# Kernel tuning notes

Hardware: AMD Instinct MI355X
Metric: run time of the kernel (lower is better)

## Reference

```python
import jax, jax.numpy as jnp
import numpy as np

N_NODES = 50000
SEQ_LEN = 32
N_TOKENS = 100000
EMB_DIM = 128          # in_feats / 2
IN_FEATS = 256
N_HIDDEN = 256
N_CLASSES = 40
N_EDGES = 800000
PAD_IX = 0


def setup_inputs() -> dict:
    key = jax.random.key(0)
    k1, k2, k3, k4, k5, k6 = jax.random.split(key, 6)
    features = jax.random.randint(k1, (N_NODES, SEQ_LEN), 0, N_TOKENS, dtype=jnp.int32)
    src = jax.random.randint(k2, (N_EDGES,), 0, N_NODES, dtype=jnp.int32)
    dst = jax.random.randint(k3, (N_EDGES,), 0, N_NODES, dtype=jnp.int32)
    emb_table = jax.random.normal(k4, (N_TOKENS, EMB_DIM), dtype=jnp.float32) * 0.02
    W1 = jax.random.normal(k5, (IN_FEATS, N_HIDDEN), dtype=jnp.float32) * 0.02
    b1 = jnp.zeros((N_HIDDEN,), dtype=jnp.float32)
    W2 = jax.random.normal(k6, (N_HIDDEN, N_CLASSES), dtype=jnp.float32) * 0.02
    b2 = jnp.zeros((N_CLASSES,), dtype=jnp.float32)
    return {"features": features, "src": src, "dst": dst,
            "emb_table": emb_table, "W1": W1, "b1": b1, "W2": W2, "b2": b2}


def _apply_embs(features, emb_table):
    # padding_idx row contributes zeros (nn.Embedding padding_idx semantics)
    emb = emb_table.at[PAD_IX].set(0.0)
    h = emb[features]                                    # [N, L, D]
    seq_len = jnp.sum(features != PAD_IX, axis=1)        # [N]
    seq_len = jnp.maximum(seq_len, 1)[:, None].astype(h.dtype)
    h1 = h.sum(axis=1) / seq_len                         # masked mean
    h2 = h.max(axis=1)                                   # max pool (pads are 0)
    return jnp.concatenate((h1, h2), axis=1)             # [N, 2D]


def _graph_conv(h, src, dst, norm_s, norm_d, W, b):
    # DGL GraphConv, norm='both': out = D_in^{-1/2} A D_out^{-1/2} h W + b
    hw = h @ W                                           # transform first (smaller msgs)
    m = (hw * norm_s[:, None])[src]                      # gather messages [E, F]
    agg = jax.ops.segment_sum(m, dst, num_segments=N_NODES)
    return agg * norm_d[:, None] + b


def reference(features, src, dst, emb_table, W1, b1, W2, b2):
    ones_e = jnp.ones((src.shape[0],), dtype=jnp.float32)
    deg_out = jnp.maximum(jax.ops.segment_sum(ones_e, src, num_segments=N_NODES), 1.0)
    deg_in = jnp.maximum(jax.ops.segment_sum(ones_e, dst, num_segments=N_NODES), 1.0)
    norm_s = deg_out ** -0.5
    norm_d = deg_in ** -0.5

    h = _apply_embs(features, emb_table)                 # [N, in_feats]
    h = jax.nn.relu(_graph_conv(h, src, dst, norm_s, norm_d, W1, b1))
    # dropout is identity in eval mode
    h = _graph_conv(h, src, dst, norm_s, norm_d, W2, b2)
    return h                                             # [N, n_classes]
```

## Files before the change

kernel.cpp:

```cpp
#include <hip/hip_runtime.h>
#include <math.h>

#define N_NODES 50000
#define SEQ_LEN 32
#define EMB_DIM 128
#define IN_FEATS 256
#define N_HIDDEN 256
#define N_CLASSES 40
#define N_EDGES 800000
#define N_TOKENS 100000

#define SLOT 64
#define NBIN 196
#define BINCAP 4608
#define EPB 4000

typedef short short8 __attribute__((ext_vector_type(8)));
typedef float f32x4 __attribute__((ext_vector_type(4)));

__device__ __forceinline__ unsigned short f2bf(float x) {
  unsigned int u = __float_as_uint(x);
  unsigned int r = (u + 0x7FFFu + ((u >> 16) & 1u)) >> 16;
  return (unsigned short)r;
}
__device__ __forceinline__ float bf2f(unsigned short s) {
  return __uint_as_float((unsigned int)s << 16);
}
__device__ __forceinline__ unsigned int pack2bf(float a, float b) {
  return (unsigned int)f2bf(a) | ((unsigned int)f2bf(b) << 16);
}

__global__ __launch_bounds__(256) void k_prep(const float* __restrict__ emb,
                                              unsigned short* __restrict__ emb_b,
                                              const float* __restrict__ W1,
                                              unsigned short* __restrict__ Wp1,
                                              const float* __restrict__ W2,
                                              unsigned short* __restrict__ Wp2) {
  int b = blockIdx.x, tid = threadIdx.x;
  if (b < 2048) {
    const int total = N_TOKENS * EMB_DIM / 4;
    for (int i = b * 256 + tid; i < total; i += 2048 * 256) {
      float4 v = ((const float4*)emb)[i];
      ushort4 o;
      o.x = f2bf(v.x); o.y = f2bf(v.y); o.z = f2bf(v.z); o.w = f2bf(v.w);
      ((ushort4*)emb_b)[i] = o;
    }
  } else if (b < 2080) {
    int g = (b - 2048) * 256 + tid;
    int lane = g & 63, jb = (g >> 6) & 15, kt = g >> 10;
    int col = jb * 16 + (lane & 15);
    int kbase = kt * 32 + (lane >> 4) * 8;
    unsigned short* o = Wp1 + (size_t)g * 8;
    #pragma unroll
    for (int e = 0; e < 8; ++e) o[e] = f2bf(W1[(size_t)(kbase + e) * N_HIDDEN + col]);
  } else {
    int g = (b - 2080) * 256 + tid;
    if (g < 8 * 3 * 64) {
      int lane = g & 63, jb = (g >> 6) % 3, kt = g / (3 * 64);
      int col = jb * 16 + (lane & 15);
      int kbase = kt * 32 + (lane >> 4) * 8;
      unsigned short* o = Wp2 + (size_t)g * 8;
      #pragma unroll
      for (int e = 0; e < 8; ++e)
        o[e] = (col < N_CLASSES) ? f2bf(W2[(size_t)(kbase + e) * N_CLASSES + col]) : (unsigned short)0;
    }
  }
}

__global__ __launch_bounds__(256) void k_binA(const int* __restrict__ src,
                                              const int* __restrict__ dst,
                                              int* __restrict__ gcntD,
                                              int* __restrict__ gcntS,
                                              unsigned int* __restrict__ dbin,
                                              unsigned char* __restrict__ sbin) {
  __shared__ int cntD[NBIN], cntS[NBIN], baseD[NBIN], baseS[NBIN];
  int tid = threadIdx.x;
  if (tid < NBIN) { cntD[tid] = 0; cntS[tid] = 0; }
  __syncthreads();
  int e0 = blockIdx.x * EPB;
  for (int j = tid; j < EPB; j += 256) {
    int d = dst[e0 + j], s = src[e0 + j];
    atomicAdd(&cntD[d >> 8], 1);
    atomicAdd(&cntS[s >> 8], 1);
  }
  __syncthreads();
  if (tid < NBIN) {
    baseD[tid] = atomicAdd(&gcntD[tid], cntD[tid]);
    baseS[tid] = atomicAdd(&gcntS[tid], cntS[tid]);
    cntD[tid] = 0;
    cntS[tid] = 0;
  }
  __syncthreads();
  for (int j = tid; j < EPB; j += 256) {
    int d = dst[e0 + j], s = src[e0 + j];
    int bd = d >> 8, bs = s >> 8;
    int od = atomicAdd(&cntD[bd], 1);
    int pd = baseD[bd] + od;
    if (pd < BINCAP) dbin[(size_t)bd * BINCAP + pd] = ((unsigned int)s << 8) | (unsigned int)(d & 255);
    int os = atomicAdd(&cntS[bs], 1);
    int ps = baseS[bs] + os;
    if (ps < BINCAP) sbin[(size_t)bs * BINCAP + ps] = (unsigned char)(s & 255);
  }
}

__global__ __launch_bounds__(256) void k_binB(const unsigned int* __restrict__ dbin,
                                              const int* __restrict__ gcntD,
                                              int* __restrict__ cursor,
                                              int* __restrict__ csr_pad) {
  __shared__ int cnt[256];
  int tid = threadIdx.x, b = blockIdx.x;
  cnt[tid] = 0;
  __syncthreads();
  int n = min(gcntD[b], BINCAP);
  const unsigned int* bb = dbin + (size_t)b * BINCAP;
  for (int j = tid; j < n; j += 256) {
    unsigned int e = bb[j];
    int lo = e & 255;
    int slot = atomicAdd(&cnt[lo], 1);
    if (slot < SLOT) csr_pad[(size_t)(b * 256 + lo) * SLOT + slot] = (int)(e >> 8);
  }
  __syncthreads();
  int node = b * 256 + tid;
  if (node < N_NODES) cursor[node] = min(cnt[tid], SLOT);
}

__global__ __launch_bounds__(256) void k_degoutnorm(const unsigned char* __restrict__ sbin,
                                                    const int* __restrict__ gcntS,
                                                    const int* __restrict__ cursor,
                                                    float* __restrict__ norm_s,
                                                    float* __restrict__ norm_d) {
  __shared__ int cnt[256];
  int tid = threadIdx.x, b = blockIdx.x;
  cnt[tid] = 0;
  __syncthreads();
  int n = min(gcntS[b], BINCAP);
  const unsigned char* bb = sbin + (size_t)b * BINCAP;
  for (int j = tid; j < n; j += 256) atomicAdd(&cnt[bb[j]], 1);
  __syncthreads();
  int node = b * 256 + tid;
  if (node < N_NODES) {
    norm_s[node] = 1.0f / sqrtf((float)max(cnt[tid], 1));
    norm_d[node] = 1.0f / sqrtf((float)max(cursor[node], 1));
  }
}

__global__ __launch_bounds__(256) void k_embed(const int* __restrict__ feats,
                                               const uint4* __restrict__ rows4,
                                               uint4* __restrict__ h4) {
  int tid = threadIdx.x;
  int w = tid >> 6, lane = tid & 63;
  int node = blockIdx.x * 4 + w;
  int lq = lane & 15, qg = lane >> 4;
  int laneL = lane & 31;

  int tok0 = feats[(size_t)node * SEQ_LEN + laneL];
  unsigned long long m = __ballot(tok0 != 0);
  int cnt = (int)__popcll(m & 0xFFFFFFFFull);
  float inv = 1.0f / (float)max(cnt, 1);

  float s0 = 0.f, s1 = 0.f, s2 = 0.f, s3 = 0.f, s4 = 0.f, s5 = 0.f, s6 = 0.f, s7 = 0.f;
  float m0 = -INFINITY, m1 = -INFINITY, m2 = -INFINITY, m3 = -INFINITY;
  float m4 = -INFINITY, m5 = -INFINITY, m6 = -INFINITY, m7 = -INFINITY;
  #pragma unroll
  for (int t = 0; t < 8; ++t) {
    int tok = __shfl(tok0, t * 4 + qg);
    uint4 v = make_uint4(0u, 0u, 0u, 0u);
    if (tok) v = rows4[(size_t)tok * 16 + lq];
    float f0 = bf2f((unsigned short)(v.x & 0xFFFF)), f1 = bf2f((unsigned short)(v.x >> 16));
    float f2 = bf2f((unsigned short)(v.y & 0xFFFF)), f3 = bf2f((unsigned short)(v.y >> 16));
    float f4 = bf2f((unsigned short)(v.z & 0xFFFF)), f5 = bf2f((unsigned short)(v.z >> 16));
    float f6 = bf2f((unsigned short)(v.w & 0xFFFF)), f7 = bf2f((unsigned short)(v.w >> 16));
    s0 += f0; s1 += f1; s2 += f2; s3 += f3; s4 += f4; s5 += f5; s6 += f6; s7 += f7;
    m0 = fmaxf(m0, f0); m1 = fmaxf(m1, f1); m2 = fmaxf(m2, f2); m3 = fmaxf(m3, f3);
    m4 = fmaxf(m4, f4); m5 = fmaxf(m5, f5); m6 = fmaxf(m6, f6); m7 = fmaxf(m7, f7);
  }
  #pragma unroll
  for (int mask = 16; mask <= 32; mask <<= 1) {
    s0 += __shfl_xor(s0, mask); s1 += __shfl_xor(s1, mask);
    s2 += __shfl_xor(s2, mask); s3 += __shfl_xor(s3, mask);
    s4 += __shfl_xor(s4, mask); s5 += __shfl_xor(s5, mask);
    s6 += __shfl_xor(s6, mask); s7 += __shfl_xor(s7, mask);
    m0 = fmaxf(m0, __shfl_xor(m0, mask)); m1 = fmaxf(m1, __shfl_xor(m1, mask));
    m2 = fmaxf(m2, __shfl_xor(m2, mask)); m3 = fmaxf(m3, __shfl_xor(m3, mask));
    m4 = fmaxf(m4, __shfl_xor(m4, mask)); m5 = fmaxf(m5, __shfl_xor(m5, mask));
    m6 = fmaxf(m6, __shfl_xor(m6, mask)); m7 = fmaxf(m7, __shfl_xor(m7, mask));
  }
  if (qg == 0) {
    uint4* hv = h4 + (size_t)node * 32;
    hv[lq] = make_uint4(pack2bf(s0 * inv, s1 * inv), pack2bf(s2 * inv, s3 * inv),
                        pack2bf(s4 * inv, s5 * inv), pack2bf(s6 * inv, s7 * inv));
    hv[16 + lq] = make_uint4(pack2bf(m0, m1), pack2bf(m2, m3),
                             pack2bf(m4, m5), pack2bf(m6, m7));
  }
}

__global__ __launch_bounds__(256) void k_mm1(const unsigned short* __restrict__ hb,
                                             const unsigned short* __restrict__ Wp,
                                             const float* __restrict__ norm_s,
                                             unsigned short* __restrict__ out) {
  __shared__ unsigned short sA[64 * 256];
  int tid = threadIdx.x;
  int r0 = blockIdx.x * 64;
  #pragma unroll
  for (int it = 0; it < 8; ++it) {
    int idx = it * 256 + tid;
    int r = idx >> 5, kb = idx & 31;
    uint4 v = make_uint4(0, 0, 0, 0);
    int row = r0 + r;
    if (row < N_NODES) v = *(const uint4*)(hb + (size_t)row * 256 + kb * 8);
    *(uint4*)&sA[r * 256 + ((kb ^ (r & 7)) << 3)] = v;
  }
  __syncthreads();

  int w = tid >> 6, lane = tid & 63;
  const short8* W8 = (const short8*)Wp;
  f32x4 acc[4][4];
  #pragma unroll
  for (int i = 0; i < 4; ++i)
    #pragma unroll
    for (int j = 0; j < 4; ++j) acc[i][j] = (f32x4){0.f, 0.f, 0.f, 0.f};

  #pragma unroll
  for (int kt = 0; kt < 8; ++kt) {
    short8 a[4], b[4];
    int kb = kt * 4 + (lane >> 4);
    #pragma unroll
    for (int ri = 0; ri < 4; ++ri) {
      int r = ri * 16 + (lane & 15);
      a[ri] = *(const short8*)&sA[r * 256 + ((kb ^ (r & 7)) << 3)];
    }
    #pragma unroll
    for (int jb = 0; jb < 4; ++jb) b[jb] = W8[(kt * 16 + w * 4 + jb) * 64 + lane];
    #pragma unroll
    for (int ri = 0; ri < 4; ++ri)
      #pragma unroll
      for (int jb = 0; jb < 4; ++jb)
        acc[ri][jb] = __builtin_amdgcn_mfma_f32_16x16x32_bf16(a[ri], b[jb], acc[ri][jb], 0, 0, 0);
  }

  #pragma unroll
  for (int ri = 0; ri < 4; ++ri) {
    #pragma unroll
    for (int rr = 0; rr < 4; ++rr) {
      int row = r0 + ri * 16 + (lane >> 4) * 4 + rr;
      if (row < N_NODES) {
        float ns = norm_s[row];
        #pragma unroll
        for (int jb = 0; jb < 4; ++jb) {
          int col = w * 64 + jb * 16 + (lane & 15);
          out[(size_t)row * 256 + col] = f2bf(acc[ri][jb][rr] * ns);
        }
      }
    }
  }
}

__global__ __launch_bounds__(256) void k_agg1(const uint4* __restrict__ rows4,
                                              const int* __restrict__ cursor,
                                              const int* __restrict__ csr_pad,
                                              const float* __restrict__ norm_d,
                                              const float* __restrict__ b1,
                                              uint4* __restrict__ out4) {
  int tid = threadIdx.x;
  int w = tid >> 6, lane = tid & 63;
  int node = blockIdx.x * 4 + w;
  int cnt = __builtin_amdgcn_readfirstlane(cursor[node]);
  const int* csr = csr_pad + (size_t)node * SLOT;
  int half = lane >> 5, lq = lane & 31;

  float a0 = 0.f, a1 = 0.f, a2 = 0.f, a3 = 0.f, a4 = 0.f, a5 = 0.f, a6 = 0.f, a7 = 0.f;
  int e = 0;
  for (; e + 8 <= cnt; e += 8) {
    int s0 = csr[e + 0 + half], s1 = csr[e + 2 + half];
    int s2 = csr[e + 4 + half], s3 = csr[e + 6 + half];
    uint4 v0 = rows4[(size_t)s0 * 32 + lq];
    uint4 v1 = rows4[(size_t)s1 * 32 + lq];
    uint4 v2 = rows4[(size_t)s2 * 32 + lq];
    uint4 v3 = rows4[(size_t)s3 * 32 + lq];
    #pragma unroll
    for (int i = 0; i < 4; ++i) {
      uint4 v = (i == 0) ? v0 : (i == 1) ? v1 : (i == 2) ? v2 : v3;
      a0 += bf2f((unsigned short)(v.x & 0xFFFF)); a1 += bf2f((unsigned short)(v.x >> 16));
      a2 += bf2f((unsigned short)(v.y & 0xFFFF)); a3 += bf2f((unsigned short)(v.y >> 16));
      a4 += bf2f((unsigned short)(v.z & 0xFFFF)); a5 += bf2f((unsigned short)(v.z >> 16));
      a6 += bf2f((unsigned short)(v.w & 0xFFFF)); a7 += bf2f((unsigned short)(v.w >> 16));
    }
  }
  for (; e + 2 <= cnt; e += 2) {
    int s = csr[e + half];
    uint4 v = rows4[(size_t)s * 32 + lq];
    a0 += bf2f((unsigned short)(v.x & 0xFFFF)); a1 += bf2f((unsigned short)(v.x >> 16));
    a2 += bf2f((unsigned short)(v.y & 0xFFFF)); a3 += bf2f((unsigned short)(v.y >> 16));
    a4 += bf2f((unsigned short)(v.z & 0xFFFF)); a5 += bf2f((unsigned short)(v.z >> 16));
    a6 += bf2f((unsigned short)(v.w & 0xFFFF)); a7 += bf2f((unsigned short)(v.w >> 16));
  }
  if (e < cnt) {
    uint4 v = make_uint4(0u, 0u, 0u, 0u);
    if (half == 0) v = rows4[(size_t)csr[e] * 32 + lq];
    a0 += bf2f((unsigned short)(v.x & 0xFFFF)); a1 += bf2f((unsigned short)(v.x >> 16));
    a2 += bf2f((unsigned short)(v.y & 0xFFFF)); a3 += bf2f((unsigned short)(v.y >> 16));
    a4 += bf2f((unsigned short)(v.z & 0xFFFF)); a5 += bf2f((unsigned short)(v.z >> 16));
    a6 += bf2f((unsigned short)(v.w & 0xFFFF)); a7 += bf2f((unsigned short)(v.w >> 16));
  }
  a0 += __shfl_xor(a0, 32); a1 += __shfl_xor(a1, 32);
  a2 += __shfl_xor(a2, 32); a3 += __shfl_xor(a3, 32);
  a4 += __shfl_xor(a4, 32); a5 += __shfl_xor(a5, 32);
  a6 += __shfl_xor(a6, 32); a7 += __shfl_xor(a7, 32);

  if (half == 0) {
    float nd = norm_d[node];
    float4 bb0 = *(const float4*)&b1[8 * lq];
    float4 bb1 = *(const float4*)&b1[8 * lq + 4];
    float o0 = fmaxf(a0 * nd + bb0.x, 0.f), o1 = fmaxf(a1 * nd + bb0.y, 0.f);
    float o2 = fmaxf(a2 * nd + bb0.z, 0.f), o3 = fmaxf(a3 * nd + bb0.w, 0.f);
    float o4 = fmaxf(a4 * nd + bb1.x, 0.f), o5 = fmaxf(a5 * nd + bb1.y, 0.f);
    float o6 = fmaxf(a6 * nd + bb1.z, 0.f), o7 = fmaxf(a7 * nd + bb1.w, 0.f);
    out4[(size_t)node * 32 + lq] = make_uint4(pack2bf(o0, o1), pack2bf(o2, o3),
                                              pack2bf(o4, o5), pack2bf(o6, o7));
  }
}

__global__ __launch_bounds__(256) void k_mm2(const unsigned short* __restrict__ h2b,
                                             const unsigned short* __restrict__ Wp,
                                             const float* __restrict__ norm_s,
                                             unsigned short* __restrict__ out) {
  __shared__ unsigned short sA[64 * 256];
  int tid = threadIdx.x;
  int r0 = blockIdx.x * 64;
  #pragma unroll
  for (int it = 0; it < 8; ++it) {
    int idx = it * 256 + tid;
    int r = idx >> 5, kb = idx & 31;
    uint4 v = make_uint4(0, 0, 0, 0);
    int row = r0 + r;
    if (row < N_NODES) v = *(const uint4*)(h2b + (size_t)row * 256 + kb * 8);
    *(uint4*)&sA[r * 256 + ((kb ^ (r & 7)) << 3)] = v;
  }
  __syncthreads();

  int w = tid >> 6, lane = tid & 63;
  const short8* W8 = (const short8*)Wp;
  f32x4 acc[3];
  #pragma unroll
  for (int j = 0; j < 3; ++j) acc[j] = (f32x4){0.f, 0.f, 0.f, 0.f};

  #pragma unroll
  for (int kt = 0; kt < 8; ++kt) {
    int r = w * 16 + (lane & 15);
    int kb = kt * 4 + (lane >> 4);
    short8 a = *(const short8*)&sA[r * 256 + ((kb ^ (r & 7)) << 3)];
    #pragma unroll
    for (int jb = 0; jb < 3; ++jb) {
      short8 b = W8[(kt * 3 + jb) * 64 + lane];
      acc[jb] = __builtin_amdgcn_mfma_f32_16x16x32_bf16(a, b, acc[jb], 0, 0, 0);
    }
  }

  #pragma unroll
  for (int rr = 0; rr < 4; ++rr) {
    int row = r0 + w * 16 + (lane >> 4) * 4 + rr;
    if (row < N_NODES) {
      float ns = norm_s[row];
      #pragma unroll
      for (int jb = 0; jb < 3; ++jb) {
        int col = jb * 16 + (lane & 15);
        if (col < N_CLASSES) out[(size_t)row * N_CLASSES + col] = f2bf(acc[jb][rr] * ns);
      }
    }
  }
}

__global__ __launch_bounds__(256) void k_agg2(const unsigned int* __restrict__ rows,
                                              const int* __restrict__ cursor,
                                              const int* __restrict__ csr_pad,
                                              const float* __restrict__ norm_d,
                                              const float* __restrict__ b2,
                                              float* __restrict__ out) {
  int tid = threadIdx.x;
  int w = tid >> 6, lane = tid & 63;
  int node = blockIdx.x * 4 + w;
  int slot = lane / 20, fl = lane % 20;
  int cnt = __builtin_amdgcn_readfirstlane(cursor[node]);
  const int* csr = csr_pad + (size_t)node * SLOT;

  float a0 = 0.f, a1 = 0.f;
  if (slot < 3) {
    for (int e = slot; e < cnt; e += 3) {
      int s = csr[e];
      unsigned int v = rows[(size_t)s * 20 + fl];
      a0 += bf2f((unsigned short)(v & 0xFFFF));
      a1 += bf2f((unsigned short)(v >> 16));
    }
  }
  float p0 = __shfl(a0, lane + 20), p1 = __shfl(a1, lane + 20);
  float q0 = __shfl(a0, lane + 40), q1 = __shfl(a1, lane + 40);
  if (slot == 0) {
    a0 += p0 + q0; a1 += p1 + q1;
    float nd = norm_d[node];
    float o0 = a0 * nd + b2[2 * fl];
    float o1 = a1 * nd + b2[2 * fl + 1];
    *(float2*)&out[(size_t)node * N_CLASSES + 2 * fl] = make_float2(o0, o1);
  }
}

extern "C" void kernel_launch(void* const* d_in, const int* in_sizes, int n_in,
                              void* d_out, int out_size, void* d_ws, size_t ws_size,
                              hipStream_t stream) {
  const int*   feats = (const int*)d_in[0];
  const int*   src   = (const int*)d_in[1];
  const int*   dst   = (const int*)d_in[2];
  const float* emb   = (const float*)d_in[3];
  const float* W1    = (const float*)d_in[4];
  const float* b1    = (const float*)d_in[5];
  const float* W2    = (const float*)d_in[6];
  const float* b2    = (const float*)d_in[7];
  float* out = (float*)d_out;

  char* base = (char*)d_ws;
  size_t off = 0;
  auto alloc = [&](size_t bytes) -> char* {
    char* p = base + off;
    off += (bytes + 255) & ~(size_t)255;
    return p;
  };
  unsigned short* hb      = (unsigned short*)alloc((size_t)N_NODES * IN_FEATS * 2);
  unsigned short* msgb    = (unsigned short*)alloc((size_t)N_NODES * N_HIDDEN * 2);
  unsigned short* hw2b    = (unsigned short*)alloc((size_t)N_NODES * N_CLASSES * 2);
  unsigned short* emb_b   = (unsigned short*)alloc((size_t)N_TOKENS * EMB_DIM * 2);
  unsigned short* Wp1     = (unsigned short*)alloc((size_t)8 * 16 * 64 * 8 * 2);
  unsigned short* Wp2     = (unsigned short*)alloc((size_t)8 * 3 * 64 * 8 * 2);
  int*   gcnt    = (int*)alloc((size_t)512 * 4);
  int*   gcntD   = gcnt;
  int*   gcntS   = gcnt + 256;
  int*   cursor  = (int*)alloc((size_t)N_NODES * 4);
  float* norm_s  = (float*)alloc((size_t)N_NODES * 4);
  float* norm_d  = (float*)alloc((size_t)N_NODES * 4);
  unsigned int*  dbin = (unsigned int*)alloc((size_t)NBIN * BINCAP * 4);
  unsigned char* sbin = (unsigned char*)alloc((size_t)NBIN * BINCAP);
  int*   csr_pad = (int*)alloc((size_t)N_NODES * SLOT * 4);

  hipMemsetAsync(gcnt, 0, 512 * 4, stream);

  k_prep<<<2086, 256, 0, stream>>>(emb, emb_b, W1, Wp1, W2, Wp2);
  k_binA<<<N_EDGES / EPB, 256, 0, stream>>>(src, dst, gcntD, gcntS, dbin, sbin);
  k_binB<<<NBIN, 256, 0, stream>>>(dbin, gcntD, cursor, csr_pad);
  k_degoutnorm<<<NBIN, 256, 0, stream>>>(sbin, gcntS, cursor, norm_s, norm_d);

  int gemm_blocks = (N_NODES + 63) / 64;
  k_embed<<<N_NODES / 4, 256, 0, stream>>>(feats, (const uint4*)emb_b, (uint4*)hb);
  k_mm1<<<gemm_blocks, 256, 0, stream>>>(hb, Wp1, norm_s, msgb);
  k_agg1<<<N_NODES / 4, 256, 0, stream>>>((const uint4*)msgb, cursor, csr_pad, norm_d, b1, (uint4*)hb);
  k_mm2<<<gemm_blocks, 256, 0, stream>>>(hb, Wp2, norm_s, hw2b);
  k_agg2<<<N_NODES / 4, 256, 0, stream>>>((const unsigned int*)hw2b, cursor, csr_pad, norm_d, b2, out);
}
```

Measured before the change: 225.8 us.

## Fuse embedding pooling into first GEMM and aggregation into second GEMM

Merges edge binning into the prep kernel and degree/CSR construction into one kernel. Embedding pooling now writes straight into the shared-memory A tile of the first MFMA GEMM, and layer-1 aggregation writes into the A tile of the second GEMM, so the intermediate h buffers no longer round-trip through global memory. norm_s scaling moves out of the mm1 epilogue, presumably into the aggregation step. The aim is fewer launches and less HBM traffic, at the cost of serial gather phases inside GEMM blocks, fewer blocks, and only half the waves doing MFMA in the second GEMM.

```diff
diff --git a/kernel.cpp b/kernel.cpp
--- a/kernel.cpp
+++ b/kernel.cpp
@@ -30,23 +30,57 @@
   return (unsigned int)f2bf(a) | ((unsigned int)f2bf(b) << 16);
 }
 
-__global__ __launch_bounds__(256) void k_prep(const float* __restrict__ emb,
-                                              unsigned short* __restrict__ emb_b,
-                                              const float* __restrict__ W1,
-                                              unsigned short* __restrict__ Wp1,
-                                              const float* __restrict__ W2,
-                                              unsigned short* __restrict__ Wp2) {
+__global__ __launch_bounds__(256) void k_pre(const int* __restrict__ src,
+                                             const int* __restrict__ dst,
+                                             int* __restrict__ gcntD,
+                                             int* __restrict__ gcntS,
+                                             unsigned int* __restrict__ dbin,
+                                             unsigned char* __restrict__ sbin,
+                                             const float* __restrict__ emb,
+                                             unsigned short* __restrict__ emb_b,
+                                             const float* __restrict__ W1,
+                                             unsigned short* __restrict__ Wp1,
+                                             const float* __restrict__ W2,
+                                             unsigned short* __restrict__ Wp2) {
+  __shared__ int cntD[NBIN], cntS[NBIN], baseD[NBIN], baseS[NBIN];
   int b = blockIdx.x, tid = threadIdx.x;
-  if (b < 2048) {
+  if (b < 200) {
+    if (tid < NBIN) { cntD[tid] = 0; cntS[tid] = 0; }
+    __syncthreads();
+    int e0 = b * EPB;
+    for (int j = tid; j < EPB; j += 256) {
+      int d = dst[e0 + j], s = src[e0 + j];
+      atomicAdd(&cntD[d >> 8], 1);
+      atomicAdd(&cntS[s >> 8], 1);
+    }
+    __syncthreads();
+    if (tid < NBIN) {
+      baseD[tid] = atomicAdd(&gcntD[tid], cntD[tid]);
+      baseS[tid] = atomicAdd(&gcntS[tid], cntS[tid]);
+      cntD[tid] = 0;
+      cntS[tid] = 0;
+    }
+    __syncthreads();
+    for (int j = tid; j < EPB; j += 256) {
+      int d = dst[e0 + j], s = src[e0 + j];
+      int bd = d >> 8, bs = s >> 8;
+      int od = atomicAdd(&cntD[bd], 1);
+      int pd = baseD[bd] + od;
+      if (pd < BINCAP) dbin[(size_t)bd * BINCAP + pd] = ((unsigned int)s << 8) | (unsigned int)(d & 255);
+      int os = atomicAdd(&cntS[bs], 1);
+      int ps = baseS[bs] + os;
+      if (ps < BINCAP) sbin[(size_t)bs * BINCAP + ps] = (unsigned char)(s & 255);
+    }
+  } else if (b < 200 + 2048) {
     const int total = N_TOKENS * EMB_DIM / 4;
-    for (int i = b * 256 + tid; i < total; i += 2048 * 256) {
+    for (int i = (b - 200) * 256 + tid; i < total; i += 2048 * 256) {
       float4 v = ((const float4*)emb)[i];
       ushort4 o;
       o.x = f2bf(v.x); o.y = f2bf(v.y); o.z = f2bf(v.z); o.w = f2bf(v.w);
       ((ushort4*)emb_b)[i] = o;
     }
-  } else if (b < 2080) {
-    int g = (b - 2048) * 256 + tid;
+  } else if (b < 200 + 2048 + 32) {
+    int g = (b - 2248) * 256 + tid;
     int lane = g & 63, jb = (g >> 6) & 15, kt = g >> 10;
     int col = jb * 16 + (lane & 15);
     int kbase = kt * 32 + (lane >> 4) * 8;
@@ -54,7 +88,7 @@
     #pragma unroll
     for (int e = 0; e < 8; ++e) o[e] = f2bf(W1[(size_t)(kbase + e) * N_HIDDEN + col]);
   } else {
-    int g = (b - 2080) * 256 + tid;
+    int g = (b - 2280) * 256 + tid;
     if (g < 8 * 3 * 64) {
       int lane = g & 63, jb = (g >> 6) % 3, kt = g / (3 * 64);
       int col = jb * 16 + (lane & 15);
@@ -67,175 +101,120 @@
   }
 }
 
-__global__ __launch_bounds__(256) void k_binA(const int* __restrict__ src,
-                                              const int* __restrict__ dst,
-                                              int* __restrict__ gcntD,
-                                              int* __restrict__ gcntS,
-                                              unsigned int* __restrict__ dbin,
-                                              unsigned char* __restrict__ sbin) {
-  __shared__ int cntD[NBIN], cntS[NBIN], baseD[NBIN], baseS[NBIN];
-  int tid = threadIdx.x;
-  if (tid < NBIN) { cntD[tid] = 0; cntS[tid] = 0; }
-  __syncthreads();
-  int e0 = blockIdx.x * EPB;
-  for (int j = tid; j < EPB; j += 256) {
-    int d = dst[e0 + j], s = src[e0 + j];
-    atomicAdd(&cntD[d >> 8], 1);
-    atomicAdd(&cntS[s >> 8], 1);
-  }
-  __syncthreads();
-  if (tid < NBIN) {
-    baseD[tid] = atomicAdd(&gcntD[tid], cntD[tid]);
-    baseS[tid] = atomicAdd(&gcntS[tid], cntS[tid]);
-    cntD[tid] = 0;
-    cntS[tid] = 0;
-  }
-  __syncthreads();
-  for (int j = tid; j < EPB; j += 256) {
-    int d = dst[e0 + j], s = src[e0 + j];
-    int bd = d >> 8, bs = s >> 8;
-    int od = atomicAdd(&cntD[bd], 1);
-    int pd = baseD[bd] + od;
-    if (pd < BINCAP) dbin[(size_t)bd * BINCAP + pd] = ((unsigned int)s << 8) | (unsigned int)(d & 255);
-    int os = atomicAdd(&cntS[bs], 1);
-    int ps = baseS[bs] + os;
-    if (ps < BINCAP) sbin[(size_t)bs * BINCAP + ps] = (unsigned char)(s & 255);
-  }
-}
-
-__global__ __launch_bounds__(256) void k_binB(const unsigned int* __restrict__ dbin,
-                                              const int* __restrict__ gcntD,
-                                              int* __restrict__ cursor,
-                                              int* __restrict__ csr_pad) {
-  __shared__ int cnt[256];
+__global__ __launch_bounds__(256) void k_graph2(const unsigned int* __restrict__ dbin,
+                                                const int* __restrict__ gcntD,
+                                                const unsigned char* __restrict__ sbin,
+                                                const int* __restrict__ gcntS,
+                                                int* __restrict__ cursor,
+                                                int* __restrict__ csr_pad,
+                                                float* __restrict__ norm_s,
+                                                float* __restrict__ norm_d) {
+  __shared__ int cntD[256], cntS[256];
   int tid = threadIdx.x, b = blockIdx.x;
-  cnt[tid] = 0;
+  cntD[tid] = 0; cntS[tid] = 0;
   __syncthreads();
   int n = min(gcntD[b], BINCAP);
   const unsigned int* bb = dbin + (size_t)b * BINCAP;
   for (int j = tid; j < n; j += 256) {
     unsigned int e = bb[j];
     int lo = e & 255;
-    int slot = atomicAdd(&cnt[lo], 1);
+    int slot = atomicAdd(&cntD[lo], 1);
     if (slot < SLOT) csr_pad[(size_t)(b * 256 + lo) * SLOT + slot] = (int)(e >> 8);
   }
-  __syncthreads();
-  int node = b * 256 + tid;
-  if (node < N_NODES) cursor[node] = min(cnt[tid], SLOT);
-}
-
-__global__ __launch_bounds__(256) void k_degoutnorm(const unsigned char* __restrict__ sbin,
-                                                    const int* __restrict__ gcntS,
-                                                    const int* __restrict__ cursor,
-                                                    float* __restrict__ norm_s,
-                                                    float* __restrict__ norm_d) {
-  __shared__ int cnt[256];
-  int tid = threadIdx.x, b = blockIdx.x;
-  cnt[tid] = 0;
-  __syncthreads();
-  int n = min(gcntS[b], BINCAP);
-  const unsigned char* bb = sbin + (size_t)b * BINCAP;
-  for (int j = tid; j < n; j += 256) atomicAdd(&cnt[bb[j]], 1);
+  int ns = min(gcntS[b], BINCAP);
+  const unsigned char* sb = sbin + (size_t)b * BINCAP;
+  for (int j = tid; j < ns; j += 256) atomicAdd(&cntS[sb[j]], 1);
   __syncthreads();
   int node = b * 256 + tid;
   if (node < N_NODES) {
-    norm_s[node] = 1.0f / sqrtf((float)max(cnt[tid], 1));
-    norm_d[node] = 1.0f / sqrtf((float)max(cursor[node], 1));
-  }
-}
-
-__global__ __launch_bounds__(256) void k_embed(const int* __restrict__ feats,
-                                               const uint4* __restrict__ rows4,
-                                               uint4* __restrict__ h4) {
+    cursor[node] = min(cntD[tid], SLOT);
+    norm_d[node] = 1.0f / sqrtf((float)max(cntD[tid], 1));
+    norm_s[node] = 1.0f / sqrtf((float)max(cntS[tid], 1));
+  }
+}
+
+__global__ __launch_bounds__(512) void k_emb_mm1(const int* __restrict__ feats,
+                                                 const uint4* __restrict__ rows4,
+                                                 const unsigned short* __restrict__ Wp,
+                                                 unsigned short* __restrict__ out) {
+  __shared__ unsigned short sA[64 * 256];
   int tid = threadIdx.x;
   int w = tid >> 6, lane = tid & 63;
-  int node = blockIdx.x * 4 + w;
-  int lq = lane & 15, qg = lane >> 4;
-  int laneL = lane & 31;
-
-  int tok0 = feats[(size_t)node * SEQ_LEN + laneL];
-  unsigned long long m = __ballot(tok0 != 0);
-  int cnt = (int)__popcll(m & 0xFFFFFFFFull);
-  float inv = 1.0f / (float)max(cnt, 1);
-
-  float s0 = 0.f, s1 = 0.f, s2 = 0.f, s3 = 0.f, s4 = 0.f, s5 = 0.f, s6 = 0.f, s7 = 0.f;
-  float m0 = -INFINITY, m1 = -INFINITY, m2 = -INFINITY, m3 = -INFINITY;
-  float m4 = -INFINITY, m5 = -INFINITY, m6 = -INFINITY, m7 = -INFINITY;
+  int r0 = blockIdx.x * 64;
+  int lq = lane & 15, qg = lane >> 4, laneL = lane & 31;
+
   #pragma unroll
-  for (int t = 0; t < 8; ++t) {
-    int tok = __shfl(tok0, t * 4 + qg);
-    uint4 v = make_uint4(0u, 0u, 0u, 0u);
-    if (tok) v = rows4[(size_t)tok * 16 + lq];
-    float f0 = bf2f((unsigned short)(v.x & 0xFFFF)), f1 = bf2f((unsigned short)(v.x >> 16));
-    float f2 = bf2f((unsigned short)(v.y & 0xFFFF)), f3 = bf2f((unsigned short)(v.y >> 16));
-    float f4 = bf2f((unsigned short)(v.z & 0xFFFF)), f5 = bf2f((unsigned short)(v.z >> 16));
-    float f6 = bf2f((unsigned short)(v.w & 0xFFFF)), f7 = bf2f((unsigned short)(v.w >> 16));
-    s0 += f0; s1 += f1; s2 += f2; s3 += f3; s4 += f4; s5 += f5; s6 += f6; s7 += f7;
-    m0 = fmaxf(m0, f0); m1 = fmaxf(m1, f1); m2 = fmaxf(m2, f2); m3 = fmaxf(m3, f3);
-    m4 = fmaxf(m4, f4); m5 = fmaxf(m5, f5); m6 = fmaxf(m6, f6); m7 = fmaxf(m7, f7);
-  }
+  for (int n = 0; n < 8; ++n) {
+    int r = w * 8 + n;
+    int node = r0 + r;
+    int tok0 = 0;
+    if (node < N_NODES) tok0 = feats[(size_t)node * SEQ_LEN + laneL];
+    unsigned long long m = __ballot(tok0 != 0);
+    int cnt = (int)__popcll(m & 0xFFFFFFFFull);
+    float inv = 1.0f / (float)max(cnt, 1);
+
+    float s0 = 0.f, s1 = 0.f, s2 = 0.f, s3 = 0.f, s4 = 0.f, s5 = 0.f, s6 = 0.f, s7 = 0.f;
+    float m0 = 0.f, m1 = 0.f, m2 = 0.f, m3 = 0.f, m4 = 0.f, m5 = 0.f, m6 = 0.f, m7 = 0.f;
+    bool first = true;
+    #pragma unroll
+    for (int t = 0; t < 8; ++t) {
+      int tok = __shfl(tok0, t * 4 + qg);
+      uint4 v = make_uint4(0u, 0u, 0u, 0u);
+      if (tok) v = rows4[(size_t)tok * 16 + lq];
+      float f0 = bf2f((unsigned short)(v.x & 0xFFFF)), f1 = bf2f((unsigned short)(v.x >> 16));
+      float f2 = bf2f((unsigned short)(v.y & 0xFFFF)), f3 = bf2f((unsigned short)(v.y >> 16));
+      float f4 = bf2f((unsigned short)(v.z & 0xFFFF)), f5 = bf2f((unsigned short)(v.z >> 16));
+      float f6 = bf2f((unsigned short)(v.w & 0xFFFF)), f7 = bf2f((unsigned short)(v.w >> 16));
+      s0 += f0; s1 += f1; s2 += f2; s3 += f3; s4 += f4; s5 += f5; s6 += f6; s7 += f7;
+      if (first) { m0 = f0; m1 = f1; m2 = f2; m3 = f3; m4 = f4; m5 = f5; m6 = f6; m7 = f7; first = false; }
+      else {
+        m0 = fmaxf(m0, f0); m1 = fmaxf(m1, f1); m2 = fmaxf(m2, f2); m3 = fmaxf(m3, f3);
+        m4 = fmaxf(m4, f4); m5 = fmaxf(m5, f5); m6 = fmaxf(m6, f6); m7 = fmaxf(m7, f7);
+      }
+    }
+    #pragma unroll
+    for (int mask = 16; mask <= 32; mask <<= 1) {
+      s0 += __shfl_xor(s0, mask); s1 += __shfl_xor(s1, mask);
+      s2 += __shfl_xor(s2, mask); s3 += __shfl_xor(s3, mask);
+      s4 += __shfl_xor(s4, mask); s5 += __shfl_xor(s5, mask);
+      s6 += __shfl_xor(s6, mask); s7 += __shfl_xor(s7, mask);
+      m0 = fmaxf(m0, __shfl_xor(m0, mask)); m1 = fmaxf(m1, __shfl_xor(m1, mask));
+      m2 = fmaxf(m2, __shfl_xor(m2, mask)); m3 = fmaxf(m3, __shfl_xor(m3, mask));
+      m4 = fmaxf(m4, __shfl_xor(m4, mask)); m5 = fmaxf(m5, __shfl_xor(m5, mask));
+      m6 = fmaxf(m6, __shfl_xor(m6, mask)); m7 = fmaxf(m7, __shfl_xor(m7, mask));
+    }
+    if (qg == 0) {
+      int kb1 = lq, kb2 = 16 + lq;
+      *(uint4*)&sA[r * 256 + ((kb1 ^ (r & 7)) << 3)] =
+          make_uint4(pack2bf(s0 * inv, s1 * inv), pack2bf(s2 * inv, s3 * inv),
+                     pack2bf(s4 * inv, s5 * inv), pack2bf(s6 * inv, s7 * inv));
+      *(uint4*)&sA[r * 256 + ((kb2 ^ (r & 7)) << 3)] =
+          make_uint4(pack2bf(m0, m1), pack2bf(m2, m3), pack2bf(m4, m5), pack2bf(m6, m7));
+    }
+  }
+  __syncthreads();
+
+  const short8* W8 = (const short8*)Wp;
+  f32x4 acc[4][2];
   #pragma unroll
-  for (int mask = 16; mask <= 32; mask <<= 1) {
-    s0 += __shfl_xor(s0, mask); s1 += __shfl_xor(s1, mask);
-    s2 += __shfl_xor(s2, mask); s3 += __shfl_xor(s3, mask);
-    s4 += __shfl_xor(s4, mask); s5 += __shfl_xor(s5, mask);
-    s6 += __shfl_xor(s6, mask); s7 += __shfl_xor(s7, mask);
-    m0 = fmaxf(m0, __shfl_xor(m0, mask)); m1 = fmaxf(m1, __shfl_xor(m1, mask));
-    m2 = fmaxf(m2, __shfl_xor(m2, mask)); m3 = fmaxf(m3, __shfl_xor(m3, mask));
-    m4 = fmaxf(m4, __shfl_xor(m4, mask)); m5 = fmaxf(m5, __shfl_xor(m5, mask));
-    m6 = fmaxf(m6, __shfl_xor(m6, mask)); m7 = fmaxf(m7, __shfl_xor(m7, mask));
-  }
-  if (qg == 0) {
-    uint4* hv = h4 + (size_t)node * 32;
-    hv[lq] = make_uint4(pack2bf(s0 * inv, s1 * inv), pack2bf(s2 * inv, s3 * inv),
-                        pack2bf(s4 * inv, s5 * inv), pack2bf(s6 * inv, s7 * inv));
-    hv[16 + lq] = make_uint4(pack2bf(m0, m1), pack2bf(m2, m3),
-                             pack2bf(m4, m5), pack2bf(m6, m7));
-  }
-}
-
-__global__ __launch_bounds__(256) void k_mm1(const unsigned short* __restrict__ hb,
-                                             const unsigned short* __restrict__ Wp,
-                                             const float* __restrict__ norm_s,
-                                             unsigned short* __restrict__ out) {
-  __shared__ unsigned short sA[64 * 256];
-  int tid = threadIdx.x;
-  int r0 = blockIdx.x * 64;
-  #pragma unroll
-  for (int it = 0; it < 8; ++it) {
-    int idx = it * 256 + tid;
-    int r = idx >> 5, kb = idx & 31;
-    uint4 v = make_uint4(0, 0, 0, 0);
-    int row = r0 + r;
-    if (row < N_NODES) v = *(const uint4*)(hb + (size_t)row * 256 + kb * 8);
-    *(uint4*)&sA[r * 256 + ((kb ^ (r & 7)) << 3)] = v;
-  }
-  __syncthreads();
-
-  int w = tid >> 6, lane = tid & 63;
-  const short8* W8 = (const short8*)Wp;
-  f32x4 acc[4][4];
-  #pragma unroll
-  for (int i = 0; i < 4; ++i)
-    #pragma unroll
-    for (int j = 0; j < 4; ++j) acc[i][j] = (f32x4){0.f, 0.f, 0.f, 0.f};
+  for (int i = 0; i < 4; ++i) { acc[i][0] = (f32x4){0.f,0.f,0.f,0.f}; acc[i][1] = (f32x4){0.f,0.f,0.f,0.f}; }
 
   #pragma unroll
   for (int kt = 0; kt < 8; ++kt) {
-    short8 a[4], b[4];
+    short8 a[4];
     int kb = kt * 4 + (lane >> 4);
     #pragma unroll
     for (int ri = 0; ri < 4; ++ri) {
       int r = ri * 16 + (lane & 15);
       a[ri] = *(const short8*)&sA[r * 256 + ((kb ^ (r & 7)) << 3)];
     }
-    #pragma unroll
-    for (int jb = 0; jb < 4; ++jb) b[jb] = W8[(kt * 16 + w * 4 + jb) * 64 + lane];
-    #pragma unroll
-    for (int ri = 0; ri < 4; ++ri)
-      #pragma unroll
-      for (int jb = 0; jb < 4; ++jb)
-        acc[ri][jb] = __builtin_amdgcn_mfma_f32_16x16x32_bf16(a[ri], b[jb], acc[ri][jb], 0, 0, 0);
+    short8 b0 = W8[(kt * 16 + w * 2 + 0) * 64 + lane];
+    short8 b1 = W8[(kt * 16 + w * 2 + 1) * 64 + lane];
+    #pragma unroll
+    for (int ri = 0; ri < 4; ++ri) {
+      acc[ri][0] = __builtin_amdgcn_mfma_f32_16x16x32_bf16(a[ri], b0, acc[ri][0], 0, 0, 0);
+      acc[ri][1] = __builtin_amdgcn_mfma_f32_16x16x32_bf16(a[ri], b1, acc[ri][1], 0, 0, 0);
+    }
   }
 
   #pragma unroll
@@ -244,127 +223,121 @@
     for (int rr = 0; rr < 4; ++rr) {
       int row = r0 + ri * 16 + (lane >> 4) * 4 + rr;
       if (row < N_NODES) {
+        #pragma unroll
+        for (int jb = 0; jb < 2; ++jb) {
+          int col = w * 32 + jb * 16 + (lane & 15);
+          out[(size_t)row * 256 + col] = f2bf(acc[ri][jb][rr]);
+        }
+      }
+    }
+  }
+}
+
+__global__ __launch_bounds__(512) void k_agg_mm2(const uint4* __restrict__ rows4,
+                                                 const int* __restrict__ cursor,
+                                                 const int* __restrict__ csr_pad,
+                                                 const float* __restrict__ norm_s,
+                                                 const float* __restrict__ norm_d,
+                                                 const float* __restrict__ b1,
+                                                 const unsigned short* __restrict__ Wp,
+                                                 unsigned short* __restrict__ out) {
+  __shared__ unsigned short sA[64 * 256];
+  int tid = threadIdx.x;
+  int w = tid >> 6, lane = tid & 63;
+  int r0 = blockIdx.x * 64;
+  int half = lane >> 5, lq = lane & 31;
+
+  #pragma unroll
+  for (int n = 0; n < 8; ++n) {
+    int r = w * 8 + n;
+    int node = r0 + r;
+    float a0 = 0.f, a1 = 0.f, a2 = 0.f, a3 = 0.f, a4 = 0.f, a5 = 0.f, a6 = 0.f, a7 = 0.f;
+    if (node < N_NODES) {
+      int cnt = __builtin_amdgcn_readfirstlane(cursor[node]);
+      const int* csr = csr_pad + (size_t)node * SLOT;
+      int e = 0;
+      for (; e + 8 <= cnt; e += 8) {
+        int s0 = csr[e + 0 + half], s1 = csr[e + 2 + half];
+        int s2 = csr[e + 4 + half], s3 = csr[e + 6 + half];
+        float ns0 = norm_s[s0], ns1 = norm_s[s1], ns2 = norm_s[s2], ns3 = norm_s[s3];
+        uint4 v0 = rows4[(size_t)s0 * 32 + lq];
+        uint4 v1 = rows4[(size_t)s1 * 32 + lq];
+        uint4 v2 = rows4[(size_t)s2 * 32 + lq];
+        uint4 v3 = rows4[(size_t)s3 * 32 + lq];
+        #pragma unroll
+        for (int i = 0; i < 4; ++i) {
+          uint4 v = (i == 0) ? v0 : (i == 1) ? v1 : (i == 2) ? v2 : v3;
+          float ns = (i == 0) ? ns0 : (i == 1) ? ns1 : (i == 2) ? ns2 : ns3;
+          a0 += ns * bf2f((unsigned short)(v.x & 0xFFFF)); a1 += ns * bf2f((unsigned short)(v.x >> 16));
+          a2 += ns * bf2f((unsigned short)(v.y & 0xFFFF)); a3 += ns * bf2f((unsigned short)(v.y >> 16));
+          a4 += ns * bf2f((unsigned short)(v.z & 0xFFFF)); a5 += ns * bf2f((unsigned short)(v.z >> 16));
+          a6 += ns * bf2f((unsigned short)(v.w & 0xFFFF)); a7 += ns * bf2f((unsigned short)(v.w >> 16));
+        }
+      }
+      for (; e + 2 <= cnt; e += 2) {
+        int s = csr[e + half];
+        float ns = norm_s[s];
+        uint4 v = rows4[(size_t)s * 32 + lq];
+        a0 += ns * bf2f((unsigned short)(v.x & 0xFFFF)); a1 += ns * bf2f((unsigned short)(v.x >> 16));
+        a2 += ns * bf2f((unsigned short)(v.y & 0xFFFF)); a3 += ns * bf2f((unsigned short)(v.y >> 16));
+        a4 += ns * bf2f((unsigned short)(v.z & 0xFFFF)); a5 += ns * bf2f((unsigned short)(v.z >> 16));
+        a6 += ns * bf2f((unsigned short)(v.w & 0xFFFF)); a7 += ns * bf2f((unsigned short)(v.w >> 16));
+      }
+      if (e < cnt && half == 0) {
+        int s = csr[e];
+        float ns = norm_s[s];
+        uint4 v = rows4[(size_t)s * 32 + lq];
+        a0 += ns * bf2f((unsigned short)(v.x & 0xFFFF)); a1 += ns * bf2f((unsigned short)(v.x >> 16));
+        a2 += ns * bf2f((unsigned short)(v.y & 0xFFFF)); a3 += ns * bf2f((unsigned short)(v.y >> 16));
+        a4 += ns * bf2f((unsigned short)(v.z & 0xFFFF)); a5 += ns * bf2f((unsigned short)(v.z >> 16));
+        a6 += ns * bf2f((unsigned short)(v.w & 0xFFFF)); a7 += ns * bf2f((unsigned short)(v.w >> 16));
+      }
+    }
+    a0 += __shfl_xor(a0, 32); a1 += __shfl_xor(a1, 32);
+    a2 += __shfl_xor(a2, 32); a3 += __shfl_xor(a3, 32);
+    a4 += __shfl_xor(a4, 32); a5 += __shfl_xor(a5, 32);
+    a6 += __shfl_xor(a6, 32); a7 += __shfl_xor(a7, 32);
+
+    if (half == 0) {
+      float nd = (node < N_NODES) ? norm_d[node] : 1.0f;
+      float4 bb0 = *(const float4*)&b1[8 * lq];
+      float4 bb1 = *(const float4*)&b1[8 * lq + 4];
+      float o0 = fmaxf(a0 * nd + bb0.x, 0.f), o1 = fmaxf(a1 * nd + bb0.y, 0.f);
+      float o2 = fmaxf(a2 * nd + bb0.z, 0.f), o3 = fmaxf(a3 * nd + bb0.w, 0.f);
+      float o4 = fmaxf(a4 * nd + bb1.x, 0.f), o5 = fmaxf(a5 * nd + bb1.y, 0.f);
+      float o6 = fmaxf(a6 * nd + bb1.z, 0.f), o7 = fmaxf(a7 * nd + bb1.w, 0.f);
+      *(uint4*)&sA[r * 256 + ((lq ^ (r & 7)) << 3)] =
+          make_uint4(pack2bf(o0, o1), pack2bf(o2, o3), pack2bf(o4, o5), pack2bf(o6, o7));
+    }
+  }
+  __syncthreads();
+
+  if (w < 4) {
+    const short8* W8 = (const short8*)Wp;
+    f32x4 acc[3];
+    #pragma unroll
+    for (int j = 0; j < 3; ++j) acc[j] = (f32x4){0.f, 0.f, 0.f, 0.f};
+    #pragma unroll
+    for (int kt = 0; kt < 8; ++kt) {
+      int r = w * 16 + (lane & 15);
+      int kb = kt * 4 + (lane >> 4);
+      short8 a = *(const short8*)&sA[r * 256 + ((kb ^ (r & 7)) << 3)];
+      #pragma unroll
+      for (int jb = 0; jb < 3; ++jb) {
+        short8 b = W8[(kt * 3 + jb) * 64 + lane];
+        acc[jb] = __builtin_amdgcn_mfma_f32_16x16x32_bf16(a, b, acc[jb], 0, 0, 0);
+      }
+    }
+    #pragma unroll
+    for (int rr = 0; rr < 4; ++rr) {
+      int row = r0 + w * 16 + (lane >> 4) * 4 + rr;
+      if (row < N_NODES) {
         float ns = norm_s[row];
         #pragma unroll
-        for (int jb = 0; jb < 4; ++jb) {
-          int col = w * 64 + jb * 16 + (lane & 15);
-          out[(size_t)row * 256 + col] = f2bf(acc[ri][jb][rr] * ns);
+        for (int jb = 0; jb < 3; ++jb) {
+          int col = jb * 16 + (lane & 15);
+          if (col < N_CLASSES) out[(size_t)row * N_CLASSES + col] = f2bf(acc[jb][rr] * ns);
         }
-      }
-    }
-  }
-}
-
-__global__ __launch_bounds__(256) void k_agg1(const uint4* __restrict__ rows4,
-                                              const int* __restrict__ cursor,
-                                              const int* __restrict__ csr_pad,
-                                              const float* __restrict__ norm_d,
-                                              const float* __restrict__ b1,
-                                              uint4* __restrict__ out4) {
-  int tid = threadIdx.x;
-  int w = tid >> 6, lane = tid & 63;
-  int node = blockIdx.x * 4 + w;
-  int cnt = __builtin_amdgcn_readfirstlane(cursor[node]);
-  const int* csr = csr_pad + (size_t)node * SLOT;
-  int half = lane >> 5, lq = lane & 31;
-
-  float a0 = 0.f, a1 = 0.f, a2 = 0.f, a3 = 0.f, a4 = 0.f, a5 = 0.f, a6 = 0.f, a7 = 0.f;
-  int e = 0;
-  for (; e + 8 <= cnt; e += 8) {
-    int s0 = csr[e + 0 + half], s1 = csr[e + 2 + half];
-    int s2 = csr[e + 4 + half], s3 = csr[e + 6 + half];
-    uint4 v0 = rows4[(size_t)s0 * 32 + lq];
-    uint4 v1 = rows4[(size_t)s1 * 32 + lq];
-    uint4 v2 = rows4[(size_t)s2 * 32 + lq];
-    uint4 v3 = rows4[(size_t)s3 * 32 + lq];
-    #pragma unroll
-    for (int i = 0; i < 4; ++i) {
-      uint4 v = (i == 0) ? v0 : (i == 1) ? v1 : (i == 2) ? v2 : v3;
-      a0 += bf2f((unsigned short)(v.x & 0xFFFF)); a1 += bf2f((unsigned short)(v.x >> 16));
-      a2 += bf2f((unsigned short)(v.y & 0xFFFF)); a3 += bf2f((unsigned short)(v.y >> 16));
-      a4 += bf2f((unsigned short)(v.z & 0xFFFF)); a5 += bf2f((unsigned short)(v.z >> 16));
-      a6 += bf2f((unsigned short)(v.w & 0xFFFF)); a7 += bf2f((unsigned short)(v.w >> 16));
-    }
-  }
-  for (; e + 2 <= cnt; e += 2) {
-    int s = csr[e + half];
-    uint4 v = rows4[(size_t)s * 32 + lq];
-    a0 += bf2f((unsigned short)(v.x & 0xFFFF)); a1 += bf2f((unsigned short)(v.x >> 16));
-    a2 += bf2f((unsigned short)(v.y & 0xFFFF)); a3 += bf2f((unsigned short)(v.y >> 16));
-    a4 += bf2f((unsigned short)(v.z & 0xFFFF)); a5 += bf2f((unsigned short)(v.z >> 16));
-    a6 += bf2f((unsigned short)(v.w & 0xFFFF)); a7 += bf2f((unsigned short)(v.w >> 16));
-  }
-  if (e < cnt) {
-    uint4 v = make_uint4(0u, 0u, 0u, 0u);
-    if (half == 0) v = rows4[(size_t)csr[e] * 32 + lq];
-    a0 += bf2f((unsigned short)(v.x & 0xFFFF)); a1 += bf2f((unsigned short)(v.x >> 16));
-    a2 += bf2f((unsigned short)(v.y & 0xFFFF)); a3 += bf2f((unsigned short)(v.y >> 16));
-    a4 += bf2f((unsigned short)(v.z & 0xFFFF)); a5 += bf2f((unsigned short)(v.z >> 16));
-    a6 += bf2f((unsigned short)(v.w & 0xFFFF)); a7 += bf2f((unsigned short)(v.w >> 16));
-  }
-  a0 += __shfl_xor(a0, 32); a1 += __shfl_xor(a1, 32);
-  a2 += __shfl_xor(a2, 32); a3 += __shfl_xor(a3, 32);
-  a4 += __shfl_xor(a4, 32); a5 += __shfl_xor(a5, 32);
-  a6 += __shfl_xor(a6, 32); a7 += __shfl_xor(a7, 32);
-
-  if (half == 0) {
-    float nd = norm_d[node];
-    float4 bb0 = *(const float4*)&b1[8 * lq];
-    float4 bb1 = *(const float4*)&b1[8 * lq + 4];
-    float o0 = fmaxf(a0 * nd + bb0.x, 0.f), o1 = fmaxf(a1 * nd + bb0.y, 0.f);
-    float o2 = fmaxf(a2 * nd + bb0.z, 0.f), o3 = fmaxf(a3 * nd + bb0.w, 0.f);
-    float o4 = fmaxf(a4 * nd + bb1.x, 0.f), o5 = fmaxf(a5 * nd + bb1.y, 0.f);
-    float o6 = fmaxf(a6 * nd + bb1.z, 0.f), o7 = fmaxf(a7 * nd + bb1.w, 0.f);
-    out4[(size_t)node * 32 + lq] = make_uint4(pack2bf(o0, o1), pack2bf(o2, o3),
-                                              pack2bf(o4, o5), pack2bf(o6, o7));
-  }
-}
-
-__global__ __launch_bounds__(256) void k_mm2(const unsigned short* __restrict__ h2b,
-                                             const unsigned short* __restrict__ Wp,
-                                             const float* __restrict__ norm_s,
-                                             unsigned short* __restrict__ out) {
-  __shared__ unsigned short sA[64 * 256];
-  int tid = threadIdx.x;
-  int r0 = blockIdx.x * 64;
-  #pragma unroll
-  for (int it = 0; it < 8; ++it) {
-    int idx = it * 256 + tid;
-    int r = idx >> 5, kb = idx & 31;
-    uint4 v = make_uint4(0, 0, 0, 0);
-    int row = r0 + r;
-    if (row < N_NODES) v = *(const uint4*)(h2b + (size_t)row * 256 + kb * 8);
-    *(uint4*)&sA[r * 256 + ((kb ^ (r & 7)) << 3)] = v;
-  }
-  __syncthreads();
-
-  int w = tid >> 6, lane = tid & 63;
-  const short8* W8 = (const short8*)Wp;
-  f32x4 acc[3];
-  #pragma unroll
-  for (int j = 0; j < 3; ++j) acc[j] = (f32x4){0.f, 0.f, 0.f, 0.f};
-
-  #pragma unroll
-  for (int kt = 0; kt < 8; ++kt) {
-    int r = w * 16 + (lane & 15);
-    int kb = kt * 4 + (lane >> 4);
-    short8 a = *(const short8*)&sA[r * 256 + ((kb ^ (r & 7)) << 3)];
-    #pragma unroll
-    for (int jb = 0; jb < 3; ++jb) {
-      short8 b = W8[(kt * 3 + jb) * 64 + lane];
-      acc[jb] = __builtin_amdgcn_mfma_f32_16x16x32_bf16(a, b, acc[jb], 0, 0, 0);
-    }
-  }
-
-  #pragma unroll
-  for (int rr = 0; rr < 4; ++rr) {
-    int row = r0 + w * 16 + (lane >> 4) * 4 + rr;
-    if (row < N_NODES) {
-      float ns = norm_s[row];
-      #pragma unroll
-      for (int jb = 0; jb < 3; ++jb) {
-        int col = jb * 16 + (lane & 15);
-        if (col < N_CLASSES) out[(size_t)row * N_CLASSES + col] = f2bf(acc[jb][rr] * ns);
       }
     }
   }
@@ -423,7 +396,6 @@
     off += (bytes + 255) & ~(size_t)255;
     return p;
   };
-  unsigned short* hb      = (unsigned short*)alloc((size_t)N_NODES * IN_FEATS * 2);
   unsigned short* msgb    = (unsigned short*)alloc((size_t)N_NODES * N_HIDDEN * 2);
   unsigned short* hw2b    = (unsigned short*)alloc((size_t)N_NODES * N_CLASSES * 2);
   unsigned short* emb_b   = (unsigned short*)alloc((size_t)N_TOKENS * EMB_DIM * 2);
@@ -441,15 +413,13 @@
 
   hipMemsetAsync(gcnt, 0, 512 * 4, stream);
 
-  k_prep<<<2086, 256, 0, stream>>>(emb, emb_b, W1, Wp1, W2, Wp2);
-  k_binA<<<N_EDGES / EPB, 256, 0, stream>>>(src, dst, gcntD, gcntS, dbin, sbin);
-  k_binB<<<NBIN, 256, 0, stream>>>(dbin, gcntD, cursor, csr_pad);
-  k_degoutnorm<<<NBIN, 256, 0, stream>>>(sbin, gcntS, cursor, norm_s, norm_d);
+  k_pre<<<200 + 2048 + 32 + 6, 256, 0, stream>>>(src, dst, gcntD, gcntS, dbin, sbin,
+                                                 emb, emb_b, W1, Wp1, W2, Wp2);
+  k_graph2<<<NBIN, 256, 0, stream>>>(dbin, gcntD, sbin, gcntS, cursor, csr_pad, norm_s, norm_d);
 
   int gemm_blocks = (N_NODES + 63) / 64;
-  k_embed<<<N_NODES / 4, 256, 0, stream>>>(feats, (const uint4*)emb_b, (uint4*)hb);
-  k_mm1<<<gemm_blocks, 256, 0, stream>>>(hb, Wp1, norm_s, msgb);
-  k_agg1<<<N_NODES / 4, 256, 0, stream>>>((const uint4*)msgb, cursor, csr_pad, norm_d, b1, (uint4*)hb);
-  k_mm2<<<gemm_blocks, 256, 0, stream>>>(hb, Wp2, norm_s, hw2b);
+  k_emb_mm1<<<gemm_blocks, 512, 0, stream>>>(feats, (const uint4*)emb_b, Wp1, msgb);
+  k_agg_mm2<<<gemm_blocks, 512, 0, stream>>>((const uint4*)msgb, cursor, csr_pad,
+                                             norm_s, norm_d, b1, Wp2, hw2b);
   k_agg2<<<N_NODES / 4, 256, 0, stream>>>((const unsigned int*)hw2b, cursor, csr_pad, norm_d, b2, out);
 }
```

Measured after the change: 230.8 us. 2.2% more time.
